# Kernel tuning notes

Measured on AMD Instinct MI355X. Metric: run time of the kernel, lower is better.

## Reference

```python
import jax, jax.numpy as jnp
import numpy as np

N_NODES = 100000
N_EDGES = 1600000
C_IN = 128
C_OUT = 128
BN_EPS = 1e-5


def setup_inputs() -> dict:
    key = jax.random.key(0)
    k = jax.random.split(key, 4)
    x = jax.random.normal(k[0], (N_NODES, C_IN), dtype=jnp.float32)
    edge_index = jax.random.randint(k[1], (2, N_EDGES), 0, N_NODES, dtype=jnp.int32)
    # nn.Linear params (Kaiming-uniform-ish scale)
    lim = 1.0 / np.sqrt(C_IN)
    W = jax.random.uniform(k[2], (C_IN, C_OUT), jnp.float32, -lim, lim)
    b = jnp.zeros((C_OUT,), jnp.float32)
    # BatchNorm (eval mode: running stats)
    gamma = jnp.ones((C_OUT,), jnp.float32)
    beta = jnp.zeros((C_OUT,), jnp.float32)
    running_mean = jnp.zeros((C_OUT,), jnp.float32)
    running_var = jnp.ones((C_OUT,), jnp.float32)
    return {"x": x, "edge_index": edge_index, "W": W, "b": b,
            "gamma": gamma, "beta": beta,
            "running_mean": running_mean, "running_var": running_var}


def reference(x, edge_index, W, b, gamma, beta, running_mean, running_var):
    # Linear projection: [N, C_in] @ [C_in, C_out]
    h = x @ W + b
    in_node, out_node = edge_index[0], edge_index[1]
    # gather edge features then scatter-mean onto destination nodes
    sums = jax.ops.segment_sum(h[in_node], out_node, num_segments=N_NODES)
    cnt = jax.ops.segment_sum(jnp.ones((in_node.shape[0],), h.dtype), out_node,
                              num_segments=N_NODES)
    agg = sums / jnp.maximum(cnt, 1.0)[:, None]  # mean; 0 for isolated nodes
    # BatchNorm1d (eval mode: running stats) + ReLU; dropout is identity in eval
    inv = jax.lax.rsqrt(running_var + BN_EPS)
    out = (agg - running_mean) * (inv * gamma) + beta
    return jax.nn.relu(out)
```

## Files before the change

kernel.cpp:

```cpp
#include <hip/hip_runtime.h>


#define NN 100000
#define NE 1600000
#define CC 128
#define BN_EPS 1e-5f
#define LBLK 1563
#define LSTR 136
#define NBUK 256
#define DPB 391
#define ACH 4096
#define ABLK 391
#define CAP 10240
#define GNB 256
#define CAP2 5120

typedef __attribute__((ext_vector_type(8))) short bf16x8;
typedef __attribute__((ext_vector_type(4))) float f32x4;

static __device__ __forceinline__ short f2bf(float f) {
  union { float f; unsigned u; } v; v.f = f;
  unsigned r = (v.u + 0x7FFF + ((v.u >> 16) & 1)) >> 16;
  return (short)r;
}
static __device__ __forceinline__ float bflo(unsigned p) {
  return __uint_as_float(p << 16);
}
static __device__ __forceinline__ float bfhi(unsigned p) {
  return __uint_as_float(p & 0xffff0000u);
}

static __device__ __forceinline__ int excl_scan256(int* a, int t, int v) {
  a[t] = v;
  __syncthreads();
  for (int d = 1; d < 256; d <<= 1) {
    const int x = (t >= d) ? a[t - d] : 0;
    __syncthreads();
    a[t] += x;
    __syncthreads();
  }
  const int incl = a[t];
  __syncthreads();
  a[t] = incl - v;
  __syncthreads();
  return incl - v;
}

__global__ __launch_bounds__(256) void prep_hist(
    const float* __restrict__ W, const float* __restrict__ bias,
    const float* __restrict__ gamma, const float* __restrict__ beta,
    const float* __restrict__ rmean, const float* __restrict__ rvar,
    const int* __restrict__ ei, short* __restrict__ Wsw,
    float* __restrict__ scsh, int* __restrict__ bhist) {
  __shared__ int lh[NBUK];
  const int t = threadIdx.x;
  const int i = blockIdx.x * 256 + t;
  if (i < CC * CC) {
    const int k = i >> 7, n = i & 127;
    const int nt = n & 7, m = n >> 3;
    const int kb = k >> 5, q = (k >> 3) & 3, j = k & 7;
    Wsw[(size_t)(((nt * 4 + kb) * 64 + (m + 16 * q)) * 8 + j)] = f2bf(W[i]);
  }
  if (i < CC) {
    const float sc = gamma[i] * rsqrtf(rvar[i] + BN_EPS);
    scsh[i] = sc;
    scsh[CC + i] = beta[i] - rmean[i] * sc;
    scsh[2 * CC + i] = bias[i];
  }
  lh[t] = 0;
  __syncthreads();
  const int e0 = blockIdx.x * ACH;
  const int e1 = min(NE, e0 + ACH);
  for (int e = e0 + t; e < e1; e += 256) atomicAdd(&lh[ei[NE + e] / DPB], 1);
  __syncthreads();
  if (lh[t]) atomicAdd(&bhist[t], lh[t]);
}

__global__ __launch_bounds__(256) void scatter_linear(
    const int* __restrict__ ei, const int* __restrict__ bhist,
    int* __restrict__ gcurz, int2* __restrict__ ebuf,
    const float* __restrict__ x, const short* __restrict__ Wsw,
    const float* __restrict__ scsh, short* __restrict__ hout,
    int scat) {
  __shared__ int2 sorted[ACH];
  __shared__ int gsc[NBUK], lh[NBUK], lex[NBUK], rb[NBUK], lc[NBUK];
  const int t = threadIdx.x;

  if (blockIdx.x < scat) {
    const int e0 = blockIdx.x * ACH;
    const int e1 = min(NE, e0 + ACH);
    const int gbase = excl_scan256(gsc, t, bhist[t]);
    lh[t] = 0;
    __syncthreads();
    for (int e = e0 + t; e < e1; e += 256) atomicAdd(&lh[ei[NE + e] / DPB], 1);
    __syncthreads();
    const int vh = lh[t];
    const int lbase = excl_scan256(lex, t, vh);
    lc[t] = lbase;
    if (vh > 0) rb[t] = gbase + atomicAdd(&gcurz[t], vh);
    __syncthreads();
    for (int e = e0 + t; e < e1; e += 256) {
      const int src = ei[e], dst = ei[NE + e];
      const int p = atomicAdd(&lc[dst / DPB], 1);
      sorted[p] = make_int2(src, dst);
    }
    __syncthreads();
    const int n = e1 - e0;
    for (int i = t; i < n; i += 256) {
      const int2 v = sorted[i];
      const int b = v.y / DPB;
      ebuf[rb[b] + (i - lex[b])] = v;
    }
    return;
  }

  short* lsA = (short*)sorted;
  const int n0 = (blockIdx.x - scat) * 64;

#pragma unroll
  for (int j = 0; j < 8; ++j) {
    const int idx = j * 256 + t;
    const int row = idx >> 5, kc4 = idx & 31;
    float4 v = make_float4(0.f, 0.f, 0.f, 0.f);
    if (n0 + row < NN) v = *(const float4*)(x + (size_t)(n0 + row) * CC + kc4 * 4);
    short4 sv;
    sv.x = f2bf(v.x); sv.y = f2bf(v.y); sv.z = f2bf(v.z); sv.w = f2bf(v.w);
    *(short4*)(lsA + row * LSTR + kc4 * 4) = sv;
  }
  __syncthreads();

  const int wave = t >> 6, lane = t & 63;
  const int quad = lane >> 4, m = lane & 15;

  f32x4 acc[8];
#pragma unroll
  for (int nt = 0; nt < 8; ++nt) acc[nt] = (f32x4){0.f, 0.f, 0.f, 0.f};

#pragma unroll
  for (int kb = 0; kb < 4; ++kb) {
    const bf16x8 a =
        *(const bf16x8*)(lsA + (wave * 16 + m) * LSTR + kb * 32 + quad * 8);
#pragma unroll
    for (int nt = 0; nt < 8; ++nt) {
      bf16x8 bb = *(const bf16x8*)(Wsw + (size_t)(((nt * 4 + kb) * 64 + lane) * 8));
      acc[nt] = __builtin_amdgcn_mfma_f32_16x16x32_bf16(a, bb, acc[nt], 0, 0, 0);
    }
  }

  const float4 b0 = *(const float4*)(scsh + 2 * CC + m * 8);
  const float4 b1 = *(const float4*)(scsh + 2 * CC + m * 8 + 4);
  const float bv[8] = {b0.x, b0.y, b0.z, b0.w, b1.x, b1.y, b1.z, b1.w};

  __syncthreads();

#pragma unroll
  for (int reg = 0; reg < 4; ++reg) {
    const int r = wave * 16 + quad * 4 + reg;
    bf16x8 hv;
#pragma unroll
    for (int nt = 0; nt < 8; ++nt) hv[nt] = f2bf(acc[nt][reg] + bv[nt]);
    *(bf16x8*)(lsA + r * LSTR + m * 8) = hv;
  }
  __syncthreads();

#pragma unroll
  for (int rr = 0; rr < 4; ++rr) {
    const int g2 = rr * 2 + (t >> 7);
    const int idx = t & 127;
    const int row = idx >> 1, half = idx & 1;
    const int R = n0 + row;
    if (R < NN) {
      bf16x8 v = *(const bf16x8*)(lsA + row * LSTR + g2 * 16 + half * 8);
      *(bf16x8*)(hout + (size_t)g2 * (NN * 16) + (size_t)R * 16 + half * 8) = v;
    }
  }
}

__global__ __launch_bounds__(1024) void bucket_to_csr(
    const int2* __restrict__ ebuf, const int* __restrict__ bhist,
    int* __restrict__ off, int* __restrict__ csr) {
  __shared__ int gs[NBUK];
  __shared__ int dh[512];
  __shared__ int s[512];
  __shared__ int lcur[512];
  __shared__ int lcsr[CAP];
  const int b = blockIdx.x, t = threadIdx.x;

  if (t < NBUK) gs[t] = bhist[t];
  __syncthreads();
  for (int d = 1; d < NBUK; d <<= 1) {
    int a0 = 0;
    if (t < NBUK && t >= d) a0 = gs[t - d];
    __syncthreads();
    if (t < NBUK) gs[t] += a0;
    __syncthreads();
  }
  const int seglen = bhist[b];
  const int segbase = gs[b] - seglen;
  const int lo = b * DPB;
  const int hi = min(NN, lo + DPB);
  const int nd = hi - lo;
  const int2* eb = ebuf + segbase;

  if (t < 512) dh[t] = 0;
  __syncthreads();
  for (int i = t; i < seglen; i += 1024) atomicAdd(&dh[eb[i].y - lo], 1);
  __syncthreads();

  if (t < 512) s[t] = dh[t];
  __syncthreads();
  for (int d = 1; d < 512; d <<= 1) {
    int a0 = 0;
    if (t < 512 && t >= d) a0 = s[t - d];
    __syncthreads();
    if (t < 512) s[t] += a0;
    __syncthreads();
  }
  if (t < 512) lcur[t] = s[t] - dh[t];
  if (t < nd) off[lo + t] = segbase + (s[t] - dh[t]);
  if (b == NBUK - 1 && t == 0) off[NN] = NE;
  __syncthreads();

  if (seglen <= CAP) {
    for (int i = t; i < seglen; i += 1024) {
      const int2 e = eb[i];
      const int p = atomicAdd(&lcur[e.y - lo], 1);
      lcsr[p] = e.x;
    }
    __syncthreads();
    for (int i = t; i < seglen; i += 1024) csr[segbase + i] = lcsr[i];
  } else {
    for (int i = t; i < seglen; i += 1024) {
      const int2 e = eb[i];
      const int p = atomicAdd(&lcur[e.y - lo], 1);
      csr[segbase + p] = e.x;
    }
  }
}

__global__ __launch_bounds__(256) void gather_bn_relu(
    const short* __restrict__ h, const int* __restrict__ off,
    const int* __restrict__ csr, const float* __restrict__ scsh,
    float* __restrict__ out) {
  __shared__ int loff[GNB + 1];
  __shared__ int lcsr[CAP2];
  const int g = blockIdx.x & 7;
  const int nb0 = (blockIdx.x >> 3) * GNB;
  const int t = threadIdx.x;
  const int nnb = min(GNB, NN - nb0);

  for (int i = t; i <= nnb; i += 256) loff[i] = off[nb0 + i];
  __syncthreads();
  const int s0 = loff[0];
  const int seglen = loff[nnb] - s0;
  const int stg = min(seglen, CAP2);
  for (int i = t; i < stg; i += 256) lcsr[i] = csr[s0 + i];
  __syncthreads();

  const int c4 = t & 3;
  const int lgid = t >> 2;
  const short* hg = h + (size_t)g * (NN * 16);
  const float4 sc = *(const float4*)(scsh + g * 16 + c4 * 4);
  const float4 sh = *(const float4*)(scsh + CC + g * 16 + c4 * 4);

  if (seglen <= CAP2) {
#pragma unroll
    for (int nn = 0; nn < 4; ++nn) {
      const int l = lgid * 4 + nn;
      if (l < nnb) {
        const int s = loff[l] - s0, e = loff[l + 1] - s0;
        float a0 = 0.f, a1 = 0.f, a2 = 0.f, a3 = 0.f;
        int i = s;
        for (; i + 4 <= e; i += 4) {
          const int e0 = lcsr[i], e1 = lcsr[i + 1];
          const int e2 = lcsr[i + 2], e3 = lcsr[i + 3];
          const uint2 p0 = *(const uint2*)(hg + (size_t)e0 * 16 + c4 * 4);
          const uint2 p1 = *(const uint2*)(hg + (size_t)e1 * 16 + c4 * 4);
          const uint2 p2 = *(const uint2*)(hg + (size_t)e2 * 16 + c4 * 4);
          const uint2 p3 = *(const uint2*)(hg + (size_t)e3 * 16 + c4 * 4);
          a0 += (bflo(p0.x) + bflo(p1.x)) + (bflo(p2.x) + bflo(p3.x));
          a1 += (bfhi(p0.x) + bfhi(p1.x)) + (bfhi(p2.x) + bfhi(p3.x));
          a2 += (bflo(p0.y) + bflo(p1.y)) + (bflo(p2.y) + bflo(p3.y));
          a3 += (bfhi(p0.y) + bfhi(p1.y)) + (bfhi(p2.y) + bfhi(p3.y));
        }
        for (; i < e; ++i) {
          const uint2 p = *(const uint2*)(hg + (size_t)lcsr[i] * 16 + c4 * 4);
          a0 += bflo(p.x); a1 += bfhi(p.x);
          a2 += bflo(p.y); a3 += bfhi(p.y);
        }
        const int node = nb0 + l;
        const float inv = (e > s) ? 1.0f / (float)(e - s) : 0.0f;
        float4 o;
        o.x = fmaxf(0.f, a0 * inv * sc.x + sh.x);
        o.y = fmaxf(0.f, a1 * inv * sc.y + sh.y);
        o.z = fmaxf(0.f, a2 * inv * sc.z + sh.z);
        o.w = fmaxf(0.f, a3 * inv * sc.w + sh.w);
        *(float4*)(out + (size_t)node * CC + g * 16 + c4 * 4) = o;
      }
    }
  } else {
    for (int nn = 0; nn < 4; ++nn) {
      const int l = lgid * 4 + nn;
      if (l < nnb) {
        const int s = loff[l], e = loff[l + 1];
        float a0 = 0.f, a1 = 0.f, a2 = 0.f, a3 = 0.f;
        for (int i = s; i < e; ++i) {
          const uint2 p = *(const uint2*)(hg + (size_t)csr[i] * 16 + c4 * 4);
          a0 += bflo(p.x); a1 += bfhi(p.x);
          a2 += bflo(p.y); a3 += bfhi(p.y);
        }
        const int node = nb0 + l;
        const float inv = (e > s) ? 1.0f / (float)(e - s) : 0.0f;
        float4 o;
        o.x = fmaxf(0.f, a0 * inv * sc.x + sh.x);
        o.y = fmaxf(0.f, a1 * inv * sc.y + sh.y);
        o.z = fmaxf(0.f, a2 * inv * sc.z + sh.z);
        o.w = fmaxf(0.f, a3 * inv * sc.w + sh.w);
        *(float4*)(out + (size_t)node * CC + g * 16 + c4 * 4) = o;
      }
    }
  }
}

__global__ __launch_bounds__(256) void edge_scatter(
    const float* __restrict__ x, const int* __restrict__ ei,
    float* __restrict__ sums, int* __restrict__ cnt) {
  int gt = blockIdx.x * 256 + threadIdx.x;
  int e = gt >> 5;
  int sub = gt & 31;
  if (e >= NE) return;
  int src = ei[e];
  int dst = ei[NE + e];
  const float4 v = *(const float4*)(x + (size_t)src * CC + sub * 4);
  float* o = sums + (size_t)dst * CC + sub * 4;
  unsafeAtomicAdd(o + 0, v.x);
  unsafeAtomicAdd(o + 1, v.y);
  unsafeAtomicAdd(o + 2, v.z);
  unsafeAtomicAdd(o + 3, v.w);
  if (sub == 0) atomicAdd(cnt + dst, 1);
}

__global__ __launch_bounds__(256) void gemm_bn_relu_fb(
    float* buf, const float* __restrict__ W, const float* __restrict__ bias,
    const float* __restrict__ gamma, const float* __restrict__ beta,
    const float* __restrict__ rmean, const float* __restrict__ rvar,
    const int* __restrict__ cnt) {
  __shared__ float xsT[CC][65];
  const int t = threadIdx.x;
  const int n0 = blockIdx.x * 64;
  for (int j = 0; j < 8; ++j) {
    int i = t + 256 * j;
    int row = i >> 5;
    int ko = (i & 31) * 4;
    float4 v = make_float4(0.f, 0.f, 0.f, 0.f);
    if (n0 + row < NN) v = *(const float4*)(buf + (size_t)(n0 + row) * CC + ko);
    xsT[ko + 0][row] = v.x;
    xsT[ko + 1][row] = v.y;
    xsT[ko + 2][row] = v.z;
    xsT[ko + 3][row] = v.w;
  }
  __syncthreads();
  const int cg = t & 31;
  const int ng8 = (t >> 5) * 8;
  float acc[8][4];
#pragma unroll
  for (int j = 0; j < 8; ++j)
#pragma unroll
    for (int c = 0; c < 4; ++c) acc[j][c] = 0.f;
#pragma unroll 8
  for (int k = 0; k < CC; ++k) {
    const float4 wv = *(const float4*)(W + k * CC + cg * 4);
#pragma unroll
    for (int j = 0; j < 8; ++j) {
      const float xv = xsT[k][ng8 + j];
      acc[j][0] = fmaf(xv, wv.x, acc[j][0]);
      acc[j][1] = fmaf(xv, wv.y, acc[j][1]);
      acc[j][2] = fmaf(xv, wv.z, acc[j][2]);
      acc[j][3] = fmaf(xv, wv.w, acc[j][3]);
    }
  }
  const float4 bb = *(const float4*)(bias + cg * 4);
  const float4 gg = *(const float4*)(gamma + cg * 4);
  const float4 bt = *(const float4*)(beta + cg * 4);
  const float4 mu = *(const float4*)(rmean + cg * 4);
  const float4 vr = *(const float4*)(rvar + cg * 4);
  float sc[4], sh[4];
  sc[0] = gg.x * rsqrtf(vr.x + BN_EPS);
  sc[1] = gg.y * rsqrtf(vr.y + BN_EPS);
  sc[2] = gg.z * rsqrtf(vr.z + BN_EPS);
  sc[3] = gg.w * rsqrtf(vr.w + BN_EPS);
  sh[0] = bt.x - mu.x * sc[0];
  sh[1] = bt.y - mu.y * sc[1];
  sh[2] = bt.z - mu.z * sc[2];
  sh[3] = bt.w - mu.w * sc[3];
#pragma unroll
  for (int j = 0; j < 8; ++j) {
    const int n = n0 + ng8 + j;
    if (n >= NN) continue;
    const int cn = cnt[n];
    const float inv = cn > 0 ? 1.0f / (float)cn : 0.0f;
    const float bsel = cn > 0 ? 1.0f : 0.0f;
    float4 o;
    o.x = fmaxf(0.f, (acc[j][0] * inv + bsel * bb.x) * sc[0] + sh[0]);
    o.y = fmaxf(0.f, (acc[j][1] * inv + bsel * bb.y) * sc[1] + sh[1]);
    o.z = fmaxf(0.f, (acc[j][2] * inv + bsel * bb.z) * sc[2] + sh[2]);
    o.w = fmaxf(0.f, (acc[j][3] * inv + bsel * bb.w) * sc[3] + sh[3]);
    *(float4*)(buf + (size_t)n * CC + cg * 4) = o;
  }
}

extern "C" void kernel_launch(void* const* d_in, const int* in_sizes, int n_in,
                              void* d_out, int out_size, void* d_ws, size_t ws_size,
                              hipStream_t stream) {
  const float* x     = (const float*)d_in[0];
  const int*   ei    = (const int*)d_in[1];
  const float* W     = (const float*)d_in[2];
  const float* bias  = (const float*)d_in[3];
  const float* gamma = (const float*)d_in[4];
  const float* beta  = (const float*)d_in[5];
  const float* rmean = (const float*)d_in[6];
  const float* rvar  = (const float*)d_in[7];
  float* out = (float*)d_out;

  const size_t OFF_B  = 0;
  const size_t BH_B   = 400128;
  const size_t GC_B   = 401152;
  const size_t CSR_B  = 802304;
  const size_t SCSH_B = 7202304;
  const size_t WSW_B  = 7204352;
  const size_t EB_B   = 7237120;
  const size_t H1_B   = 20037120;
  const size_t NEED1  = H1_B + (size_t)NN * CC * 2;
  const size_t NEED2  = EB_B + (size_t)NN * CC * 2;

  const int GGRID = ((NN + GNB - 1) / GNB) * 8;

  if (ws_size >= NEED2) {
    int*   off   = (int*)((char*)d_ws + OFF_B);
    int*   bhist = (int*)((char*)d_ws + BH_B);
    int*   gcurz = (int*)((char*)d_ws + GC_B);
    int*   csr   = (int*)((char*)d_ws + CSR_B);
    float* scsh  = (float*)((char*)d_ws + SCSH_B);
    short* Wsw   = (short*)((char*)d_ws + WSW_B);

    hipMemsetAsync(bhist, 0, 2048, stream);
    prep_hist<<<ABLK, 256, 0, stream>>>(W, bias, gamma, beta, rmean, rvar,
                                        ei, Wsw, scsh, bhist);
    if (ws_size >= NEED1) {
      int2*  ebuf = (int2*)((char*)d_ws + EB_B);
      short* h    = (short*)((char*)d_ws + H1_B);
      scatter_linear<<<ABLK + LBLK, 256, 0, stream>>>(
          ei, bhist, gcurz, ebuf, x, Wsw, scsh, h, ABLK);
      bucket_to_csr<<<NBUK, 1024, 0, stream>>>(ebuf, bhist, off, csr);
      gather_bn_relu<<<GGRID, 256, 0, stream>>>(h, off, csr, scsh, out);
    } else {
      int2*  ebuf = (int2*)((char*)d_ws + EB_B);
      short* h    = (short*)((char*)d_ws + EB_B);
      scatter_linear<<<ABLK, 256, 0, stream>>>(
          ei, bhist, gcurz, ebuf, x, Wsw, scsh, h, ABLK);
      bucket_to_csr<<<NBUK, 1024, 0, stream>>>(ebuf, bhist, off, csr);
      scatter_linear<<<LBLK, 256, 0, stream>>>(
          ei, bhist, gcurz, ebuf, x, Wsw, scsh, h, 0);
      gather_bn_relu<<<GGRID, 256, 0, stream>>>(h, off, csr, scsh, out);
    }
  } else {
    int* cnt = (int*)d_ws;
    hipMemsetAsync(out, 0, (size_t)NN * CC * sizeof(float), stream);
    hipMemsetAsync(cnt, 0, (size_t)NN * sizeof(int), stream);
    edge_scatter<<<(NE * 32) / 256, 256, 0, stream>>>(x, ei, out, cnt);
    gemm_bn_relu_fb<<<(NN + 63) / 64, 256, 0, stream>>>(
        out, W, bias, gamma, beta, rmean, rvar, cnt);
  }
}
```

Before: 238.7 us.

## Parallelize gather across edges per node with wave-level shuffle reduction

```diff
diff --git a/kernel.cpp b/kernel.cpp
--- a/kernel.cpp
+++ b/kernel.cpp
@@ -257,66 +257,66 @@
   for (int i = t; i < stg; i += 256) lcsr[i] = csr[s0 + i];
   __syncthreads();
 
-  const int c4 = t & 3;
-  const int lgid = t >> 2;
-  const short* hg = h + (size_t)g * (NN * 16);
-  const float4 sc = *(const float4*)(scsh + g * 16 + c4 * 4);
-  const float4 sh = *(const float4*)(scsh + CC + g * 16 + c4 * 4);
-
+  const int wave = t >> 6, lane = t & 63;
+  const int el = lane & 7;
+  const int c8 = lane >> 3;
+  const unsigned* hb = (const unsigned*)(h + (size_t)g * (NN * 16)) + c8;
+  const float2 sc = *(const float2*)(scsh + g * 16 + c8 * 2);
+  const float2 sh = *(const float2*)(scsh + CC + g * 16 + c8 * 2);
+
+  const int lEnd = min(nnb, wave * 64 + 64);
   if (seglen <= CAP2) {
-#pragma unroll
-    for (int nn = 0; nn < 4; ++nn) {
-      const int l = lgid * 4 + nn;
-      if (l < nnb) {
-        const int s = loff[l] - s0, e = loff[l + 1] - s0;
-        float a0 = 0.f, a1 = 0.f, a2 = 0.f, a3 = 0.f;
-        int i = s;
-        for (; i + 4 <= e; i += 4) {
-          const int e0 = lcsr[i], e1 = lcsr[i + 1];
-          const int e2 = lcsr[i + 2], e3 = lcsr[i + 3];
-          const uint2 p0 = *(const uint2*)(hg + (size_t)e0 * 16 + c4 * 4);
-          const uint2 p1 = *(const uint2*)(hg + (size_t)e1 * 16 + c4 * 4);
-          const uint2 p2 = *(const uint2*)(hg + (size_t)e2 * 16 + c4 * 4);
-          const uint2 p3 = *(const uint2*)(hg + (size_t)e3 * 16 + c4 * 4);
-          a0 += (bflo(p0.x) + bflo(p1.x)) + (bflo(p2.x) + bflo(p3.x));
-          a1 += (bfhi(p0.x) + bfhi(p1.x)) + (bfhi(p2.x) + bfhi(p3.x));
-          a2 += (bflo(p0.y) + bflo(p1.y)) + (bflo(p2.y) + bflo(p3.y));
-          a3 += (bfhi(p0.y) + bfhi(p1.y)) + (bfhi(p2.y) + bfhi(p3.y));
-        }
-        for (; i < e; ++i) {
-          const uint2 p = *(const uint2*)(hg + (size_t)lcsr[i] * 16 + c4 * 4);
-          a0 += bflo(p.x); a1 += bfhi(p.x);
-          a2 += bflo(p.y); a3 += bfhi(p.y);
-        }
-        const int node = nb0 + l;
-        const float inv = (e > s) ? 1.0f / (float)(e - s) : 0.0f;
-        float4 o;
-        o.x = fmaxf(0.f, a0 * inv * sc.x + sh.x);
-        o.y = fmaxf(0.f, a1 * inv * sc.y + sh.y);
-        o.z = fmaxf(0.f, a2 * inv * sc.z + sh.z);
-        o.w = fmaxf(0.f, a3 * inv * sc.w + sh.w);
-        *(float4*)(out + (size_t)node * CC + g * 16 + c4 * 4) = o;
+    for (int l = wave * 64; l < lEnd; ++l) {
+      const int s = loff[l] - s0, en = loff[l + 1] - s0;
+      float ax = 0.f, ay = 0.f;
+      int i = s + el;
+      for (; i + 8 < en; i += 16) {
+        const int q0 = lcsr[i], q1 = lcsr[i + 8];
+        const unsigned p0 = hb[(size_t)q0 * 8];
+        const unsigned p1 = hb[(size_t)q1 * 8];
+        ax += bflo(p0) + bflo(p1);
+        ay += bfhi(p0) + bfhi(p1);
+      }
+      if (i < en) {
+        const unsigned p = hb[(size_t)lcsr[i] * 8];
+        ax += bflo(p); ay += bfhi(p);
+      }
+      ax += __shfl_xor(ax, 1); ay += __shfl_xor(ay, 1);
+      ax += __shfl_xor(ax, 2); ay += __shfl_xor(ay, 2);
+      ax += __shfl_xor(ax, 4); ay += __shfl_xor(ay, 4);
+      if (el == 0) {
+        const float inv = (en > s) ? 1.0f / (float)(en - s) : 0.0f;
+        float2 o;
+        o.x = fmaxf(0.f, ax * inv * sc.x + sh.x);
+        o.y = fmaxf(0.f, ay * inv * sc.y + sh.y);
+        *(float2*)(out + (size_t)(nb0 + l) * CC + g * 16 + c8 * 2) = o;
       }
     }
   } else {
-    for (int nn = 0; nn < 4; ++nn) {
-      const int l = lgid * 4 + nn;
-      if (l < nnb) {
-        const int s = loff[l], e = loff[l + 1];
-        float a0 = 0.f, a1 = 0.f, a2 = 0.f, a3 = 0.f;
-        for (int i = s; i < e; ++i) {
-          const uint2 p = *(const uint2*)(hg + (size_t)csr[i] * 16 + c4 * 4);
-          a0 += bflo(p.x); a1 += bfhi(p.x);
-          a2 += bflo(p.y); a3 += bfhi(p.y);
-        }
-        const int node = nb0 + l;
-        const float inv = (e > s) ? 1.0f / (float)(e - s) : 0.0f;
-        float4 o;
-        o.x = fmaxf(0.f, a0 * inv * sc.x + sh.x);
-        o.y = fmaxf(0.f, a1 * inv * sc.y + sh.y);
-        o.z = fmaxf(0.f, a2 * inv * sc.z + sh.z);
-        o.w = fmaxf(0.f, a3 * inv * sc.w + sh.w);
-        *(float4*)(out + (size_t)node * CC + g * 16 + c4 * 4) = o;
+    for (int l = wave * 64; l < lEnd; ++l) {
+      const int s = loff[l], en = loff[l + 1];
+      float ax = 0.f, ay = 0.f;
+      int i = s + el;
+      for (; i + 8 < en; i += 16) {
+        const int q0 = csr[i], q1 = csr[i + 8];
+        const unsigned p0 = hb[(size_t)q0 * 8];
+        const unsigned p1 = hb[(size_t)q1 * 8];
+        ax += bflo(p0) + bflo(p1);
+        ay += bfhi(p0) + bfhi(p1);
+      }
+      if (i < en) {
+        const unsigned p = hb[(size_t)csr[i] * 8];
+        ax += bflo(p); ay += bfhi(p);
+      }
+      ax += __shfl_xor(ax, 1); ay += __shfl_xor(ay, 1);
+      ax += __shfl_xor(ax, 2); ay += __shfl_xor(ay, 2);
+      ax += __shfl_xor(ax, 4); ay += __shfl_xor(ay, 4);
+      if (el == 0) {
+        const float inv = (en > s) ? 1.0f / (float)(en - s) : 0.0f;
+        float2 o;
+        o.x = fmaxf(0.f, ax * inv * sc.x + sh.x);
+        o.y = fmaxf(0.f, ay * inv * sc.y + sh.y);
+        *(float2*)(out + (size_t)(nb0 + l) * CC + g * 16 + c8 * 2) = o;
       }
     }
   }
```

Result: slower. 296.9 us (+24.4%).
